# Kernel tuning notes

Measured on AMD Instinct MI355X. Metric: run time of the kernel, lower is better.

## Reference

```python
import jax, jax.numpy as jnp
import numpy as np

B, N, H = 4, 200, 300


def setup_inputs() -> dict:
    key = jax.random.key(0)
    ks = jax.random.split(key, 6)
    s = 1.0 / np.sqrt(H)
    return {
        "x": jax.random.normal(ks[0], (B, N, H), dtype=jnp.float32),
        "e": jax.random.normal(ks[1], (B, N, N, H), dtype=jnp.float32),
        "U_w": jax.random.uniform(ks[2], (H, H), jnp.float32, -s, s),
        "U_b": jax.random.uniform(ks[3], (H,), jnp.float32, -s, s),
        "V_w": jax.random.uniform(ks[4], (H, H), jnp.float32, -s, s),
        "V_b": jax.random.uniform(ks[5], (H,), jnp.float32, -s, s),
    }


def reference(x, e, U_w, U_b, V_w, V_b):
    # Ue = e @ U_w.T + U_b  -> (B, N, N, H)
    Ue = jnp.einsum("bijh,gh->bijg", e, U_w) + U_b
    # Vx = x @ V_w.T + V_b  -> (B, N, H)
    Vx = jnp.einsum("bnh,gh->bng", x, V_w) + V_b
    # e_new[b,i,j] = Ue[b,i,j] + Vx[b,i] + Vx[b,j]
    e_new = Ue + Vx[:, :, None, :] + Vx[:, None, :, :]
    return e_new
```

## Files before the change

kernel.cpp:

```cpp
#include <hip/hip_runtime.h>
#include <hip/hip_bf16.h>

#define BB 4
#define NN 200
#define HH 300
#define NCH 10
#define GF 20
#define BM 64

typedef __attribute__((ext_vector_type(8))) short short8;
typedef __attribute__((ext_vector_type(4))) float float4v;

static __device__ __forceinline__ ushort f2bf(float x) {
    union { float f; uint u; } v; v.f = x;
    uint r = v.u + 0x7FFFu + ((v.u >> 16) & 1u);
    return (ushort)(r >> 16);
}

static __device__ __forceinline__ short8 pack8_cvt(float4v a, float4v b) {
    uint u0, u1, u2, u3;
    asm("v_cvt_pk_bf16_f32 %0, %1, %2" : "=v"(u0) : "v"(a[0]), "v"(a[1]));
    asm("v_cvt_pk_bf16_f32 %0, %1, %2" : "=v"(u1) : "v"(a[2]), "v"(a[3]));
    asm("v_cvt_pk_bf16_f32 %0, %1, %2" : "=v"(u2) : "v"(b[0]), "v"(b[1]));
    asm("v_cvt_pk_bf16_f32 %0, %1, %2" : "=v"(u3) : "v"(b[2]), "v"(b[3]));
    union { uint u[4]; short8 s; } r;
    r.u[0] = u0; r.u[1] = u1; r.u[2] = u2; r.u[3] = u3;
    return r.s;
}

static __device__ __forceinline__ void gload_lds16(const void* g, void* l) {
    __builtin_amdgcn_global_load_lds(
        (const __attribute__((address_space(1))) unsigned int*)g,
        (__attribute__((address_space(3))) unsigned int*)l, 16, 0, 0);
}

__global__ void pack_u(const float* __restrict__ Uw, ushort* __restrict__ Bp) {
    int idx = blockIdx.x * 256 + threadIdx.x;
    if (idx >= NCH * GF * 64) return;
    int lane = idx & 63;
    int kg = idx >> 6;
    int gf = kg % GF, ks = kg / GF;
    int g = gf * 16 + (lane & 15);
    int h0 = ks * 32 + (lane >> 4) * 8;
    ushort v[8];
#pragma unroll
    for (int j = 0; j < 8; ++j) {
        int h = h0 + j;
        v[j] = (g < HH && h < HH) ? f2bf(Uw[g * HH + h]) : (ushort)0;
    }
    *reinterpret_cast<short8*>(Bp + (size_t)idx * 8) = *reinterpret_cast<const short8*>(v);
}

__global__ void vx_kernel(const float* __restrict__ x, const float* __restrict__ Vw,
                          const float* __restrict__ Vb, const float* __restrict__ Ub,
                          float* __restrict__ Vx) {
    __shared__ float xs[HH];
    int row = blockIdx.x;
    const float* xr = x + (size_t)row * HH;
    for (int h = threadIdx.x; h < HH; h += 256) xs[h] = xr[h];
    __syncthreads();
    for (int g = threadIdx.x; g < HH; g += 256) {
        const float4* wr = reinterpret_cast<const float4*>(Vw + (size_t)g * HH);
        const float4* xv = reinterpret_cast<const float4*>(xs);
        float s0 = 0.f, s1 = 0.f, s2 = 0.f, s3 = 0.f;
#pragma unroll 5
        for (int k = 0; k < HH / 4; ++k) {
            float4 w = wr[k];
            float4 xx = xv[k];
            s0 += w.x * xx.x; s1 += w.y * xx.y; s2 += w.z * xx.z; s3 += w.w * xx.w;
        }
        Vx[(size_t)row * HH + g] = Vb[g] + 0.5f * Ub[g] + s0 + s1 + s2 + s3;
    }
}

__launch_bounds__(256, 3)
__global__ void gemm_kernel(const float* __restrict__ e, const ushort* __restrict__ Bp,
                            const float* __restrict__ Vx, float* __restrict__ out) {
    __shared__ __align__(16) ushort Blds[2][GF * 512];
    const int tid = threadIdx.x;
    const int w = tid >> 6, l = tid & 63;
    const int r = l & 15, q = l >> 4;
    const int m0 = blockIdx.x * BM;
    const float* rowp = e + (size_t)(m0 + w * 16 + r) * HH;

    float4v acc[GF];
#pragma unroll
    for (int f = 0; f < GF; ++f) acc[f] = (float4v){0.f, 0.f, 0.f, 0.f};

    float4v e0a, e0b, e1a, e1b;

#define LOAD_A(K_, S_) do {                                                     \
        int c0_ = (K_) * 32 + q * 8;                                            \
        const float* p0_ = (c0_ + 4 <= HH) ? rowp + c0_ : e;                    \
        const float* p1_ = (c0_ + 8 <= HH) ? rowp + c0_ + 4 : e;                \
        S_##a = *reinterpret_cast<const float4v*>(p0_);                         \
        S_##b = *reinterpret_cast<const float4v*>(p1_);                         \
    } while (0)

#define STAGE_B(K_, P_) do {                                                    \
        const char* bs_ = (const char*)Bp + (size_t)(K_) * (GF * 1024);         \
        char* bd_ = (char*)&Blds[P_][0];                                        \
        _Pragma("unroll")                                                       \
        for (int rd_ = 0; rd_ < 5; ++rd_)                                       \
            gload_lds16(bs_ + rd_ * 4096 + tid * 16, bd_ + rd_ * 4096 + tid * 16); \
    } while (0)

#define COMPUTE(K_, P_, S_) do {                                                \
        short8 fa_ = pack8_cvt(S_##a, S_##b);                                   \
        if ((K_) == 9) {                                                        \
            int c0_ = 288 + q * 8;                                              \
            _Pragma("unroll")                                                   \
            for (int j_ = 0; j_ < 8; ++j_)                                      \
                if (c0_ + j_ >= HH) fa_[j_] = 0;                                \
        }                                                                       \
        const ushort* bb_ = &Blds[P_][l * 8];                                   \
        _Pragma("unroll")                                                       \
        for (int f_ = 0; f_ < GF; ++f_) {                                       \
            short8 bf_ = *reinterpret_cast<const short8*>(bb_ + f_ * 512);      \
            acc[f_] = __builtin_amdgcn_mfma_f32_16x16x32_bf16(bf_, fa_, acc[f_], 0, 0, 0); \
        }                                                                       \
    } while (0)

#define ENDPHASE() do {                                                         \
        __builtin_amdgcn_sched_barrier(0);                                      \
        asm volatile("s_waitcnt vmcnt(0)" ::: "memory");                        \
        __builtin_amdgcn_s_barrier();                                           \
        __builtin_amdgcn_sched_barrier(0);                                      \
    } while (0)

    STAGE_B(0, 0); LOAD_A(0, e0);
    ENDPHASE();

#define PHASE(T_, P_, SC_, SN_) do {                                            \
        if ((T_) < 9) { STAGE_B((T_) + 1, (P_) ^ 1); LOAD_A((T_) + 1, SN_); }   \
        COMPUTE(T_, P_, SC_);                                                   \
        if ((T_) < 9) ENDPHASE();                                               \
    } while (0)

    PHASE(0, 0, e0, e1);
    PHASE(1, 1, e1, e0);
    PHASE(2, 0, e0, e1);
    PHASE(3, 1, e1, e0);
    PHASE(4, 0, e0, e1);
    PHASE(5, 1, e1, e0);
    PHASE(6, 0, e0, e1);
    PHASE(7, 1, e1, e0);
    PHASE(8, 0, e0, e1);
    PHASE(9, 1, e1, e0);

    {
        const int m = m0 + w * 16 + r;
        int j = m % NN;
        int ti = m / NN;
        int b = ti / NN;
        const float* vi = Vx + (size_t)ti * HH;
        const float* vj = Vx + (size_t)(b * NN + j) * HH;
        float* orow = out + (size_t)m * HH;
#pragma unroll
        for (int f = 0; f < GF - 1; ++f) {
            int g0 = f * 16 + q * 4;
            if (g0 + 4 <= HH) {
                float4v vi4 = *reinterpret_cast<const float4v*>(vi + g0);
                float4v vj4 = *reinterpret_cast<const float4v*>(vj + g0);
                *reinterpret_cast<float4v*>(orow + g0) = acc[f] + vi4 + vj4;
            }
        }
    }
#undef LOAD_A
#undef STAGE_B
#undef COMPUTE
#undef ENDPHASE
#undef PHASE
}

extern "C" void kernel_launch(void* const* d_in, const int* in_sizes, int n_in,
                              void* d_out, int out_size, void* d_ws, size_t ws_size,
                              hipStream_t stream) {
    const float* x  = (const float*)d_in[0];
    const float* e  = (const float*)d_in[1];
    const float* Uw = (const float*)d_in[2];
    const float* Ub = (const float*)d_in[3];
    const float* Vw = (const float*)d_in[4];
    const float* Vb = (const float*)d_in[5];
    float* out = (float*)d_out;

    ushort* Bp = (ushort*)d_ws;
    float*  Vx = (float*)((char*)d_ws + 204800);

    pack_u<<<50, 256, 0, stream>>>(Uw, Bp);
    vx_kernel<<<BB * NN, 256, 0, stream>>>(x, Vw, Vb, Ub, Vx);
    gemm_kernel<<<160000 / BM, 256, 0, stream>>>(e, Bp, Vx, out);
}
```

Before: 160.9 us.

## Double K-chunk to 64 and keep two stages of loads in flight

Each pipeline phase now covers 64 columns of K instead of 32, so the loop has 5 phases instead of 10. The kernel issues loads for the next two chunks before computing and waits with a partial vmcnt rather than draining all outstanding memory operations. The goal is to keep more global loads of e and U in flight and to halve the number of barriers. In exchange, LDS use doubles and the launch bound drops from 3 to 2 blocks per CU, which lowers occupancy and may reduce latency hiding from other warps.

```diff
diff --git a/kernel.cpp b/kernel.cpp
--- a/kernel.cpp
+++ b/kernel.cpp
@@ -4,7 +4,6 @@
 #define BB 4
 #define NN 200
 #define HH 300
-#define NCH 10
 #define GF 20
 #define BM 64
 
@@ -36,7 +35,7 @@
 
 __global__ void pack_u(const float* __restrict__ Uw, ushort* __restrict__ Bp) {
     int idx = blockIdx.x * 256 + threadIdx.x;
-    if (idx >= NCH * GF * 64) return;
+    if (idx >= 10 * GF * 64) return;
     int lane = idx & 63;
     int kg = idx >> 6;
     int gf = kg % GF, ks = kg / GF;
@@ -73,10 +72,10 @@
     }
 }
 
-__launch_bounds__(256, 3)
+__launch_bounds__(256, 2)
 __global__ void gemm_kernel(const float* __restrict__ e, const ushort* __restrict__ Bp,
                             const float* __restrict__ Vx, float* __restrict__ out) {
-    __shared__ __align__(16) ushort Blds[2][GF * 512];
+    __shared__ __align__(16) ushort Blds[2][20480];
     const int tid = threadIdx.x;
     const int w = tid >> 6, l = tid & 63;
     const int r = l & 15, q = l >> 4;
@@ -87,66 +86,76 @@
 #pragma unroll
     for (int f = 0; f < GF; ++f) acc[f] = (float4v){0.f, 0.f, 0.f, 0.f};
 
-    float4v e0a, e0b, e1a, e1b;
-
-#define LOAD_A(K_, S_) do {                                                     \
-        int c0_ = (K_) * 32 + q * 8;                                            \
-        const float* p0_ = (c0_ + 4 <= HH) ? rowp + c0_ : e;                    \
-        const float* p1_ = (c0_ + 8 <= HH) ? rowp + c0_ + 4 : e;                \
-        S_##a = *reinterpret_cast<const float4v*>(p0_);                         \
-        S_##b = *reinterpret_cast<const float4v*>(p1_);                         \
-    } while (0)
-
-#define STAGE_B(K_, P_) do {                                                    \
-        const char* bs_ = (const char*)Bp + (size_t)(K_) * (GF * 1024);         \
+    float4v s0a0, s0a1, s0b0, s0b1, s1a0, s1a1, s1b0, s1b1;
+
+#define LOAD_A(KC_, S_) do {                                                    \
+        int ca_ = (KC_) * 64 + q * 8;                                           \
+        int cb_ = ca_ + 32;                                                     \
+        const float* pa0_ = (ca_ + 4 <= HH) ? rowp + ca_ : e;                   \
+        const float* pa1_ = (ca_ + 8 <= HH) ? rowp + ca_ + 4 : e;               \
+        const float* pb0_ = (cb_ + 4 <= HH) ? rowp + cb_ : e;                   \
+        const float* pb1_ = (cb_ + 8 <= HH) ? rowp + cb_ + 4 : e;               \
+        S_##a0 = *reinterpret_cast<const float4v*>(pa0_);                       \
+        S_##a1 = *reinterpret_cast<const float4v*>(pa1_);                       \
+        S_##b0 = *reinterpret_cast<const float4v*>(pb0_);                       \
+        S_##b1 = *reinterpret_cast<const float4v*>(pb1_);                       \
+    } while (0)
+
+#define STAGE_B(KC_, P_) do {                                                   \
+        const char* bs_ = (const char*)Bp + (size_t)(KC_) * 40960;              \
         char* bd_ = (char*)&Blds[P_][0];                                        \
         _Pragma("unroll")                                                       \
-        for (int rd_ = 0; rd_ < 5; ++rd_)                                       \
+        for (int rd_ = 0; rd_ < 10; ++rd_)                                      \
             gload_lds16(bs_ + rd_ * 4096 + tid * 16, bd_ + rd_ * 4096 + tid * 16); \
     } while (0)
 
-#define COMPUTE(K_, P_, S_) do {                                                \
-        short8 fa_ = pack8_cvt(S_##a, S_##b);                                   \
-        if ((K_) == 9) {                                                        \
+#define COMPUTE(KC_, P_, S_) do {                                               \
+        short8 fa0_ = pack8_cvt(S_##a0, S_##a1);                                \
+        short8 fa1_ = pack8_cvt(S_##b0, S_##b1);                                \
+        if ((KC_) == 4) {          \
             int c0_ = 288 + q * 8;                                              \
             _Pragma("unroll")                                                   \
             for (int j_ = 0; j_ < 8; ++j_)                                      \
-                if (c0_ + j_ >= HH) fa_[j_] = 0;                                \
+                if (c0_ + j_ >= HH) fa1_[j_] = 0;                               \
         }                                                                       \
         const ushort* bb_ = &Blds[P_][l * 8];                                   \
         _Pragma("unroll")                                                       \
         for (int f_ = 0; f_ < GF; ++f_) {                                       \
             short8 bf_ = *reinterpret_cast<const short8*>(bb_ + f_ * 512);      \
-            acc[f_] = __builtin_amdgcn_mfma_f32_16x16x32_bf16(bf_, fa_, acc[f_], 0, 0, 0); \
+            acc[f_] = __builtin_amdgcn_mfma_f32_16x16x32_bf16(bf_, fa0_, acc[f_], 0, 0, 0); \
         }                                                                       \
-    } while (0)
-
-#define ENDPHASE() do {                                                         \
+        _Pragma("unroll")                                                       \
+        for (int f_ = 0; f_ < GF; ++f_) {                                       \
+            short8 bf_ = *reinterpret_cast<const short8*>(bb_ + 10240 + f_ * 512); \
+            acc[f_] = __builtin_amdgcn_mfma_f32_16x16x32_bf16(bf_, fa1_, acc[f_], 0, 0, 0); \
+        }                                                                       \
+    } while (0)
+
+#define WAITV(N_) do {                                                          \
         __builtin_amdgcn_sched_barrier(0);                                      \
-        asm volatile("s_waitcnt vmcnt(0)" ::: "memory");                        \
+        asm volatile("s_waitcnt vmcnt(" #N_ ")" ::: "memory");                  \
+        __builtin_amdgcn_sched_barrier(0);                                      \
+    } while (0)
+
+#define BARX() do {                                                             \
+        asm volatile("s_waitcnt lgkmcnt(0)" ::: "memory");                      \
         __builtin_amdgcn_s_barrier();                                           \
         __builtin_amdgcn_sched_barrier(0);                                      \
     } while (0)
 
-    STAGE_B(0, 0); LOAD_A(0, e0);
-    ENDPHASE();
-
-#define PHASE(T_, P_, SC_, SN_) do {                                            \
-        if ((T_) < 9) { STAGE_B((T_) + 1, (P_) ^ 1); LOAD_A((T_) + 1, SN_); }   \
-        COMPUTE(T_, P_, SC_);                                                   \
-        if ((T_) < 9) ENDPHASE();                                               \
-    } while (0)
-
-    PHASE(0, 0, e0, e1);
-    PHASE(1, 1, e1, e0);
-    PHASE(2, 0, e0, e1);
-    PHASE(3, 1, e1, e0);
-    PHASE(4, 0, e0, e1);
-    PHASE(5, 1, e1, e0);
-    PHASE(6, 0, e0, e1);
-    PHASE(7, 1, e1, e0);
-    PHASE(8, 0, e0, e1);
-    PHASE(9, 1, e1, e0);
+    STAGE_B(0, 0); LOAD_A(0, s0);
+    STAGE_B(1, 1); LOAD_A(1, s1);
+    WAITV(14); BARX();
+
+    COMPUTE(0, 0, s0); BARX();
+    STAGE_B(2, 0); LOAD_A(2, s0); WAITV(14); BARX();
+    COMPUTE(1, 1, s1); BARX();
+    STAGE_B(3, 1); LOAD_A(3, s1); WAITV(14); BARX();
+    COMPUTE(2, 0, s0); BARX();
+    STAGE_B(4, 0); LOAD_A(4, s0); WAITV(14); BARX();
+    COMPUTE(3, 1, s1); BARX();
+    WAITV(0); BARX();
+    COMPUTE(4, 0, s0);
 
     {
         const int m = m0 + w * 16 + r;
@@ -169,8 +178,8 @@
 #undef LOAD_A
 #undef STAGE_B
 #undef COMPUTE
-#undef ENDPHASE
-#undef PHASE
+#undef WAITV
+#undef BARX
 }
 
 extern "C" void kernel_launch(void* const* d_in, const int* in_sizes, int n_in,
```

After: 151.6 us. 1.06x faster.
